# Kernel tuning notes

Hardware: AMD Instinct MI355X
Metric: run time of the kernel (lower is better)

The kernel has to match this reference:

```python
import jax, jax.numpy as jnp
import numpy as np
import math

N_EMBD = 1024
N_HEAD = 16
HEAD_DIM = N_EMBD // N_HEAD
# Faithful to source: scores = QK^T / scale, where scale = 1/sqrt(head_dim)
# => scores = QK^T * sqrt(head_dim)
INV_SCALE = math.sqrt(HEAD_DIM)


def setup_inputs() -> dict:
    key = jax.random.key(0)
    ks = jax.random.split(key, 9)
    B, S = 4, 2048
    x = jax.random.normal(ks[0], (B, S, N_EMBD), dtype=jnp.float32)
    init = 1.0 / math.sqrt(N_EMBD)
    def lin(kw, kb):
        W = jax.random.uniform(kw, (N_EMBD, N_EMBD), jnp.float32, -init, init)
        b = jax.random.uniform(kb, (N_EMBD,), jnp.float32, -init, init)
        return W, b
    Wq, bq = lin(ks[1], ks[2])
    Wk, bk = lin(ks[3], ks[4])
    Wv, bv = lin(ks[5], ks[6])
    Wo, bo = lin(ks[7], ks[8])
    return {"x": x, "Wq": Wq, "bq": bq, "Wk": Wk, "bk": bk,
            "Wv": Wv, "bv": bv, "Wo": Wo, "bo": bo}


def reference(x, Wq, bq, Wk, bk, Wv, bv, Wo, bo):
    B, S, _ = x.shape
    # projections (torch Linear: y = x @ W^T + b; here weights stored [in,out])
    q = (x @ Wq + bq).reshape(B, S, N_HEAD, HEAD_DIM)
    k = (x @ Wk + bk).reshape(B, S, N_HEAD, HEAD_DIM)
    v = (x @ Wv + bv).reshape(B, S, N_HEAD, HEAD_DIM)
    # scores: [B, H, S, S]; note unusual scaling (divide by 1/sqrt(d))
    scores = jnp.einsum('bqhd,bkhd->bhqk', q, k) * INV_SCALE
    attn = jax.nn.softmax(scores, axis=-1)
    # dropout in eval mode -> identity
    out = jnp.einsum('bhqk,bkhd->bqhd', attn, v).reshape(B, S, N_EMBD)
    return out @ Wo + bo
```

## Files before the change

kernel.cpp:

```cpp
#include <hip/hip_runtime.h>
#include <hip/hip_bf16.h>

#define DEVI static __device__ __forceinline__

typedef __attribute__((ext_vector_type(8))) _Float16 f16x8;
typedef __attribute__((ext_vector_type(2))) __fp16 fp16v2;
typedef __attribute__((ext_vector_type(4))) float f32x4;
typedef __attribute__((ext_vector_type(16))) float f32x16;
typedef __attribute__((ext_vector_type(8))) unsigned short u16x8;
typedef __attribute__((ext_vector_type(4))) unsigned int u32x4;
typedef __attribute__((ext_vector_type(2))) unsigned int u32x2;
typedef unsigned short u16;

constexpr int NE = 1024;
constexpr int NH = 16;
constexpr int HD = 64;
constexpr int SB = 4;
constexpr int SS = 2048;
constexpr int MR = SB * SS;

DEVI u16 f2h(float f) {
  union { _Float16 h; u16 u; } x;
  x.h = (_Float16)f;
  return x.u;
}

DEVI unsigned pk2(float lo, float hi) {
  union { fp16v2 h2; unsigned u; } cv;
  cv.h2 = __builtin_amdgcn_cvt_pkrtz(lo, hi);
  return cv.u;
}

DEVI void gload_lds16(const void* g, void* l) {
  __builtin_amdgcn_global_load_lds(
      (const __attribute__((address_space(1))) unsigned int*)g,
      (__attribute__((address_space(3))) unsigned int*)l, 16, 0, 0);
}

__global__ void k_cvt_x(const float* __restrict__ x, u16* __restrict__ xb) {
  size_t i = (size_t)blockIdx.x * 256 + threadIdx.x;
  const f32x4* s4 = (const f32x4*)x;
  f32x4 a = s4[2 * i], c = s4[2 * i + 1];
  u16x8 o;
  o[0] = f2h(a[0]); o[1] = f2h(a[1]); o[2] = f2h(a[2]); o[3] = f2h(a[3]);
  o[4] = f2h(c[0]); o[5] = f2h(c[1]); o[6] = f2h(c[2]); o[7] = f2h(c[3]);
  ((u16x8*)xb)[i] = o;
}

__global__ void k_wt(const float* __restrict__ W0, const float* __restrict__ W1,
                     const float* __restrict__ W2, const float* __restrict__ W3,
                     u16* __restrict__ WT) {
  __shared__ float tile[64][65];
  const float* W = (blockIdx.z == 0) ? W0 : (blockIdx.z == 1) ? W1 : (blockIdx.z == 2) ? W2 : W3;
  u16* T = WT + (size_t)blockIdx.z * NE * NE;
  int tid = threadIdx.x, c = tid & 63, rr = tid >> 6;
  int ti = blockIdx.y * 64, tj = blockIdx.x * 64;
#pragma unroll
  for (int p = 0; p < 16; p++) {
    int r = p * 4 + rr;
    tile[r][c] = W[(size_t)(ti + r) * NE + tj + c];
  }
  __syncthreads();
#pragma unroll
  for (int p = 0; p < 16; p++) {
    int r = p * 4 + rr;
    T[(size_t)(tj + r) * NE + ti + c] = f2h(tile[c][r]);
  }
}

template <int MODE>
__global__ __launch_bounds__(256) void k_gemm(const u16* __restrict__ A,
                                              const u16* __restrict__ BT,
                                              const float* __restrict__ bias,
                                              void* __restrict__ outp) {
  __shared__ __align__(16) u16 lA[128 * 64];
  __shared__ __align__(16) u16 lB[128 * 64];
  const int tid = threadIdx.x;
  const int wave = tid >> 6, lane = tid & 63;
  const int wr = wave >> 1, wc = wave & 1;
  const int fr = lane & 15, fg = lane >> 4;
  const int srow = lane >> 3;
  const int scol = ((lane & 7) ^ srow) * 8;
  const int mb = blockIdx.x, nb = blockIdx.y;
  f32x4 acc[4][4] = {};
  for (int kt = 0; kt < NE / 64; ++kt) {
#pragma unroll
    for (int p = 0; p < 4; p++) {
      int rb = wave * 32 + p * 8;
      gload_lds16(A + (size_t)(mb * 128 + rb + srow) * NE + kt * 64 + scol, lA + rb * 64);
      gload_lds16(BT + (size_t)(nb * 128 + rb + srow) * NE + kt * 64 + scol, lB + rb * 64);
    }
    __syncthreads();
#pragma unroll
    for (int kd = 0; kd < 2; ++kd) {
      f16x8 af[4], bg[4];
#pragma unroll
      for (int mi = 0; mi < 4; mi++) {
        int row = wr * 64 + mi * 16 + fr;
        af[mi] = *(const f16x8*)((const char*)lA + row * 128 + ((kd * 64 + fg * 16) ^ ((row & 7) << 4)));
      }
#pragma unroll
      for (int nj = 0; nj < 4; nj++) {
        int row = wc * 64 + nj * 16 + fr;
        bg[nj] = *(const f16x8*)((const char*)lB + row * 128 + ((kd * 64 + fg * 16) ^ ((row & 7) << 4)));
      }
#pragma unroll
      for (int mi = 0; mi < 4; mi++)
#pragma unroll
        for (int nj = 0; nj < 4; nj++)
          acc[mi][nj] = __builtin_amdgcn_mfma_f32_16x16x32_f16(af[mi], bg[nj], acc[mi][nj], 0, 0, 0);
    }
    __syncthreads();
  }
  float bv[4];
#pragma unroll
  for (int nj = 0; nj < 4; nj++) bv[nj] = bias[nb * 128 + wc * 64 + nj * 16 + fr];
#pragma unroll
  for (int mi = 0; mi < 4; mi++)
#pragma unroll
    for (int nj = 0; nj < 4; nj++)
#pragma unroll
      for (int r = 0; r < 4; r++) {
        int row = mb * 128 + wr * 64 + mi * 16 + fg * 4 + r;
        int col = nb * 128 + wc * 64 + nj * 16 + fr;
        float v = acc[mi][nj][r] + bv[nj];
        if constexpr (MODE == 2) {
          ((float*)outp)[(size_t)row * NE + col] = v;
        } else if constexpr (MODE == 0) {
          ((u16*)outp)[(size_t)row * NE + col] = f2h(v);
        } else {
          int b = row >> 11, s = row & (SS - 1);
          int h = col >> 6, d = col & 63;
          ((u16*)outp)[(((size_t)(b * NH + h) * HD + d) << 11) | (size_t)s] = f2h(v);
        }
      }
}

__global__ __launch_bounds__(256) void k_attn(const u16* __restrict__ Q, const u16* __restrict__ K,
                                              const u16* __restrict__ VT, u16* __restrict__ AO) {
  __shared__ __align__(16) u16 smem[6 * 4096];
  const int tid = threadIdx.x, wave = tid >> 6, lane = tid & 63;
  const int q32 = lane & 31, hh = lane >> 5;
  const int srow = lane >> 3;
  const int scol = ((lane & 7) ^ srow) * 8;
  const int bid = blockIdx.x;
  const int xcd = bid & 7, idx = bid >> 3;
  const int g = xcd * 8 + (idx >> 4);
  const int qb = (idx & 15) * 128;
  const int b = g >> 4, h = g & 15;
  const u16* Kg = K + (size_t)(b * SS) * NE + h * HD;
  const u16* Vg = VT + (size_t)(b * NH + h) * HD * SS;
  const u16* Qp = Q + (size_t)(b * SS + qb + wave * 32 + q32) * NE + h * HD;
  f16x8 qf[4];
#pragma unroll
  for (int m = 0; m < 4; m++) qf[m] = *(const f16x8*)(Qp + m * 16 + hh * 8);
  f32x16 oacc[2] = {};
  float m_s = -1e30f, l_s = 0.f;
  const float SC = 8.0f * 1.44269504088896340736f;

  auto STAGE = [&](int kt2, int bufi) {
    u16* lk = smem + bufi * 4096;
    u16* lv = smem + 12288 + bufi * 4096;
#pragma unroll
    for (int p = 0; p < 2; p++) {
      int rb = wave * 16 + p * 8;
      gload_lds16(Kg + (size_t)(kt2 * 64 + rb + srow) * NE + scol, lk + rb * 64);
      gload_lds16(Vg + (size_t)(rb + srow) * SS + kt2 * 64 + scol, lv + rb * 64);
    }
  };

  auto QK = [&](int bufi, f32x16* s) {
    const u16* lk = smem + bufi * 4096;
#pragma unroll
    for (int kt32 = 0; kt32 < 2; kt32++) {
      f32x16 z = {};
      int row = kt32 * 32 + q32;
      __builtin_amdgcn_s_setprio(1);
#pragma unroll
      for (int m = 0; m < 4; m++) {
        f16x8 kf = *(const f16x8*)((const char*)lk + row * 128 + ((m * 32 + hh * 16) ^ ((row & 7) << 4)));
        z = __builtin_amdgcn_mfma_f32_32x32x16_f16(kf, qf[m], z, 0, 0, 0);
      }
      __builtin_amdgcn_s_setprio(0);
      s[kt32] = z;
    }
  };

  auto SMPV = [&](int bufiV, f32x16* s) {
    const u16* lv = smem + 12288 + bufiV * 4096;
    float a[16];
#pragma unroll
    for (int r = 0; r < 16; r++) a[r] = fmaxf(s[0][r], s[1][r]);
#pragma unroll
    for (int st = 8; st > 0; st >>= 1)
#pragma unroll
      for (int r = 0; r < st; r++) a[r] = fmaxf(a[r], a[r + st]);
    float mx = a[0] * SC;
    mx = fmaxf(mx, __shfl_xor(mx, 32));
    float mo = m_s, mu = mo;
    if (!__all(mx <= mo + 8.f)) {
      float nm = fmaxf(mo, mx);
      float fs = __builtin_amdgcn_exp2f(mo - nm);
      m_s = nm; mu = nm; l_s *= fs;
#pragma unroll
      for (int d2 = 0; d2 < 2; d2++)
#pragma unroll
        for (int r = 0; r < 16; r++) oacc[d2][r] *= fs;
    }
    float p[2][16];
#pragma unroll
    for (int kt32 = 0; kt32 < 2; kt32++)
#pragma unroll
      for (int r = 0; r < 16; r++)
        p[kt32][r] = __builtin_amdgcn_exp2f(s[kt32][r] * SC - mu);
    float t[16];
#pragma unroll
    for (int r = 0; r < 16; r++) t[r] = p[0][r] + p[1][r];
#pragma unroll
    for (int st = 8; st > 0; st >>= 1)
#pragma unroll
      for (int r = 0; r < st; r++) t[r] += t[r + st];
    float rs = t[0];
    rs += __shfl_xor(rs, 32);
    l_s += rs;
    unsigned bw[4][4];
#pragma unroll
    for (int kt32 = 0; kt32 < 2; kt32++)
#pragma unroll
      for (int tau = 0; tau < 2; tau++)
#pragma unroll
        for (int b2 = 0; b2 < 2; b2++) {
          unsigned Y = pk2(p[kt32][4 * (2 * tau) + 2 * b2],     p[kt32][4 * (2 * tau) + 2 * b2 + 1]);
          unsigned X = pk2(p[kt32][4 * (2 * tau + 1) + 2 * b2], p[kt32][4 * (2 * tau + 1) + 2 * b2 + 1]);
          u32x2 r2 = __builtin_amdgcn_permlane32_swap(Y, X, false, false);
          int tt = kt32 * 2 + tau;
          bw[tt][b2]     = r2[0];
          bw[tt][b2 + 2] = r2[1];
        }
    f16x8 pf[4];
#pragma unroll
    for (int tt = 0; tt < 4; tt++) {
      union { unsigned w[4]; f16x8 v; } u;
#pragma unroll
      for (int w = 0; w < 4; w++) u.w[w] = bw[tt][w];
      pf[tt] = u.v;
    }
#pragma unroll
    for (int d2 = 0; d2 < 2; d2++) {
      int row = d2 * 32 + q32;
      __builtin_amdgcn_s_setprio(1);
#pragma unroll
      for (int tt = 0; tt < 4; tt++) {
        f16x8 vf = *(const f16x8*)((const char*)lv + row * 128 + ((tt * 32 + hh * 16) ^ ((row & 7) << 4)));
        oacc[d2] = __builtin_amdgcn_mfma_f32_32x32x16_f16(vf, pf[tt], oacc[d2], 0, 0, 0);
      }
      __builtin_amdgcn_s_setprio(0);
    }
  };

  f32x16 s[2];
  STAGE(0, 0);
  STAGE(1, 1);
  for (int kt = 0; kt < 32; ++kt) {
    const int cur = kt % 3;
    if (kt < 30) asm volatile("s_waitcnt vmcnt(4)" ::: "memory");
    else         asm volatile("s_waitcnt vmcnt(0)" ::: "memory");
    __builtin_amdgcn_s_barrier();
    __builtin_amdgcn_sched_barrier(0);
    if (kt + 2 < 32) STAGE(kt + 2, (kt + 2) % 3);
    QK(cur, s);
    SMPV(cur, s);
  }

  __syncthreads();
  unsigned* epi = (unsigned*)smem + wave * (32 * 36);
  float inv = 1.0f / l_s;
#pragma unroll
  for (int d2 = 0; d2 < 2; d2++)
#pragma unroll
    for (int aa = 0; aa < 4; aa++)
#pragma unroll
      for (int b2 = 0; b2 < 2; b2++) {
        int r0 = 4 * aa + 2 * b2;
        epi[q32 * 36 + d2 * 16 + 4 * aa + 2 * hh + b2] =
            pk2(oacc[d2][r0] * inv, oacc[d2][r0 + 1] * inv);
      }
  __syncthreads();
  {
    int q2 = lane >> 1, part = lane & 1;
    const unsigned* src = (const unsigned*)smem + wave * (32 * 36) + q2 * 36 + part * 16;
    u16* dst = AO + (size_t)(b * SS + qb + wave * 32 + q2) * NE + h * HD + part * 32;
#pragma unroll
    for (int u = 0; u < 4; u++)
      *(u32x4*)(dst + u * 8) = *(const u32x4*)(src + u * 4);
  }
}

extern "C" void kernel_launch(void* const* d_in, const int* in_sizes, int n_in,
                              void* d_out, int out_size, void* d_ws, size_t ws_size,
                              hipStream_t stream) {
  const float* x  = (const float*)d_in[0];
  const float* Wq = (const float*)d_in[1]; const float* bq = (const float*)d_in[2];
  const float* Wk = (const float*)d_in[3]; const float* bk = (const float*)d_in[4];
  const float* Wv = (const float*)d_in[5]; const float* bv = (const float*)d_in[6];
  const float* Wo = (const float*)d_in[7]; const float* bo = (const float*)d_in[8];

  u16* xb  = (u16*)d_ws;
  u16* WT  = xb  + (size_t)MR * NE;
  u16* Qb  = WT  + (size_t)4 * NE * NE;
  u16* Kb  = Qb  + (size_t)MR * NE;
  u16* VTb = Kb  + (size_t)MR * NE;
  u16* AOb = xb;

  k_cvt_x<<<dim3(MR * NE / (256 * 8)), 256, 0, stream>>>(x, xb);
  k_wt<<<dim3(16, 16, 4), 256, 0, stream>>>(Wq, Wk, Wv, Wo, WT);

  dim3 gg(MR / 128, NE / 128);
  k_gemm<0><<<gg, 256, 0, stream>>>(xb, WT + 0 * (size_t)NE * NE, bq, Qb);
  k_gemm<0><<<gg, 256, 0, stream>>>(xb, WT + 1 * (size_t)NE * NE, bk, Kb);
  k_gemm<1><<<gg, 256, 0, stream>>>(xb, WT + 2 * (size_t)NE * NE, bv, VTb);

  k_attn<<<dim3(1024), 256, 0, stream>>>(Qb, Kb, VTb, AOb);

  k_gemm<2><<<gg, 256, 0, stream>>>(AOb, WT + 3 * (size_t)NE * NE, bo, (float*)d_out);
}
```

Before: 225.0 us.

## Fuse QKV projections into one GEMM launch and read K/V directly from global

The three Q/K/V projection GEMMs become a single launch with a 24-column grid, where each block picks its bias and output buffer by segment. This removes two kernel launches and gives more blocks per wave. The attention kernel drops its LDS triple-buffered K/V staging pipeline and loads K and V fragments straight from global memory inside the MFMA loops, keeping LDS only for the epilogue. That removes barriers and LDS traffic, but it exposes global-memory latency and loses the cross-wave sharing of K/V tiles.

After: 371.5 us. 65.1% more time.

```diff
diff --git a/kernel.cpp b/kernel.cpp
--- a/kernel.cpp
+++ b/kernel.cpp
@@ -123,26 +123,88 @@
       for (int r = 0; r < 4; r++) {
         int row = mb * 128 + wr * 64 + mi * 16 + fg * 4 + r;
         int col = nb * 128 + wc * 64 + nj * 16 + fr;
-        float v = acc[mi][nj][r] + bv[nj];
-        if constexpr (MODE == 2) {
-          ((float*)outp)[(size_t)row * NE + col] = v;
-        } else if constexpr (MODE == 0) {
-          ((u16*)outp)[(size_t)row * NE + col] = f2h(v);
+        ((float*)outp)[(size_t)row * NE + col] = acc[mi][nj][r] + bv[nj];
+      }
+}
+
+__global__ __launch_bounds__(256) void k_gemm_qkv(const u16* __restrict__ A,
+                                                  const u16* __restrict__ BT,
+                                                  const float* __restrict__ bq,
+                                                  const float* __restrict__ bk,
+                                                  const float* __restrict__ bv,
+                                                  u16* __restrict__ Qb,
+                                                  u16* __restrict__ Kb,
+                                                  u16* __restrict__ VTb) {
+  __shared__ __align__(16) u16 lA[128 * 64];
+  __shared__ __align__(16) u16 lB[128 * 64];
+  const int tid = threadIdx.x;
+  const int wave = tid >> 6, lane = tid & 63;
+  const int wr = wave >> 1, wc = wave & 1;
+  const int fr = lane & 15, fg = lane >> 4;
+  const int srow = lane >> 3;
+  const int scol = ((lane & 7) ^ srow) * 8;
+  const int mb = blockIdx.x, nb = blockIdx.y;
+  const int seg = nb >> 3;
+  const float* bias = (seg == 0) ? bq : (seg == 1) ? bk : bv;
+  u16* outO = (seg == 0) ? Qb : (seg == 1) ? Kb : VTb;
+  f32x4 acc[4][4] = {};
+  for (int kt = 0; kt < NE / 64; ++kt) {
+#pragma unroll
+    for (int p = 0; p < 4; p++) {
+      int rb = wave * 32 + p * 8;
+      gload_lds16(A + (size_t)(mb * 128 + rb + srow) * NE + kt * 64 + scol, lA + rb * 64);
+      gload_lds16(BT + (size_t)(nb * 128 + rb + srow) * NE + kt * 64 + scol, lB + rb * 64);
+    }
+    __syncthreads();
+#pragma unroll
+    for (int kd = 0; kd < 2; ++kd) {
+      f16x8 af[4], bg[4];
+#pragma unroll
+      for (int mi = 0; mi < 4; mi++) {
+        int row = wr * 64 + mi * 16 + fr;
+        af[mi] = *(const f16x8*)((const char*)lA + row * 128 + ((kd * 64 + fg * 16) ^ ((row & 7) << 4)));
+      }
+#pragma unroll
+      for (int nj = 0; nj < 4; nj++) {
+        int row = wc * 64 + nj * 16 + fr;
+        bg[nj] = *(const f16x8*)((const char*)lB + row * 128 + ((kd * 64 + fg * 16) ^ ((row & 7) << 4)));
+      }
+#pragma unroll
+      for (int mi = 0; mi < 4; mi++)
+#pragma unroll
+        for (int nj = 0; nj < 4; nj++)
+          acc[mi][nj] = __builtin_amdgcn_mfma_f32_16x16x32_f16(af[mi], bg[nj], acc[mi][nj], 0, 0, 0);
+    }
+    __syncthreads();
+  }
+  const int colb = (nb & 7) * 128;
+  float bvv[4];
+#pragma unroll
+  for (int nj = 0; nj < 4; nj++) bvv[4 - 4 + nj] = bias[colb + wc * 64 + nj * 16 + fr];
+#pragma unroll
+  for (int mi = 0; mi < 4; mi++)
+#pragma unroll
+    for (int nj = 0; nj < 4; nj++)
+#pragma unroll
+      for (int r = 0; r < 4; r++) {
+        int row = mb * 128 + wr * 64 + mi * 16 + fg * 4 + r;
+        int col = colb + wc * 64 + nj * 16 + fr;
+        float v = acc[mi][nj][r] + bvv[nj];
+        if (seg < 2) {
+          outO[(size_t)row * NE + col] = f2h(v);
         } else {
           int b = row >> 11, s = row & (SS - 1);
           int h = col >> 6, d = col & 63;
-          ((u16*)outp)[(((size_t)(b * NH + h) * HD + d) << 11) | (size_t)s] = f2h(v);
+          outO[(((size_t)(b * NH + h) * HD + d) << 11) | (size_t)s] = f2h(v);
         }
       }
 }
 
 __global__ __launch_bounds__(256) void k_attn(const u16* __restrict__ Q, const u16* __restrict__ K,
                                               const u16* __restrict__ VT, u16* __restrict__ AO) {
-  __shared__ __align__(16) u16 smem[6 * 4096];
+  __shared__ unsigned epi_s[4][32 * 36];
   const int tid = threadIdx.x, wave = tid >> 6, lane = tid & 63;
   const int q32 = lane & 31, hh = lane >> 5;
-  const int srow = lane >> 3;
-  const int scol = ((lane & 7) ^ srow) * 8;
   const int bid = blockIdx.x;
   const int xcd = bid & 7, idx = bid >> 3;
   const int g = xcd * 8 + (idx >> 4);
@@ -157,37 +219,24 @@
   f32x16 oacc[2] = {};
   float m_s = -1e30f, l_s = 0.f;
   const float SC = 8.0f * 1.44269504088896340736f;
-
-  auto STAGE = [&](int kt2, int bufi) {
-    u16* lk = smem + bufi * 4096;
-    u16* lv = smem + 12288 + bufi * 4096;
-#pragma unroll
-    for (int p = 0; p < 2; p++) {
-      int rb = wave * 16 + p * 8;
-      gload_lds16(Kg + (size_t)(kt2 * 64 + rb + srow) * NE + scol, lk + rb * 64);
-      gload_lds16(Vg + (size_t)(rb + srow) * SS + kt2 * 64 + scol, lv + rb * 64);
-    }
-  };
-
-  auto QK = [&](int bufi, f32x16* s) {
-    const u16* lk = smem + bufi * 4096;
+  const u16* Kp = Kg + (size_t)q32 * NE + hh * 8;
+  const u16* Vp0 = Vg + (size_t)q32 * SS + hh * 8;
+
+  for (int kt = 0; kt < 32; ++kt) {
+    f32x16 s[2];
 #pragma unroll
     for (int kt32 = 0; kt32 < 2; kt32++) {
       f32x16 z = {};
-      int row = kt32 * 32 + q32;
+      const u16* kp = Kp + (size_t)(kt * 64 + kt32 * 32) * NE;
       __builtin_amdgcn_s_setprio(1);
 #pragma unroll
       for (int m = 0; m < 4; m++) {
-        f16x8 kf = *(const f16x8*)((const char*)lk + row * 128 + ((m * 32 + hh * 16) ^ ((row & 7) << 4)));
+        f16x8 kf = *(const f16x8*)(kp + m * 16);
         z = __builtin_amdgcn_mfma_f32_32x32x16_f16(kf, qf[m], z, 0, 0, 0);
       }
       __builtin_amdgcn_s_setprio(0);
       s[kt32] = z;
     }
-  };
-
-  auto SMPV = [&](int bufiV, f32x16* s) {
-    const u16* lv = smem + 12288 + bufiV * 4096;
     float a[16];
 #pragma unroll
     for (int r = 0; r < 16; r++) a[r] = fmaxf(s[0][r], s[1][r]);
@@ -247,33 +296,18 @@
     }
 #pragma unroll
     for (int d2 = 0; d2 < 2; d2++) {
-      int row = d2 * 32 + q32;
+      const u16* vp = Vp0 + (size_t)(d2 * 32) * SS + kt * 64;
       __builtin_amdgcn_s_setprio(1);
 #pragma unroll
       for (int tt = 0; tt < 4; tt++) {
-        f16x8 vf = *(const f16x8*)((const char*)lv + row * 128 + ((tt * 32 + hh * 16) ^ ((row & 7) << 4)));
+        f16x8 vf = *(const f16x8*)(vp + tt * 16);
         oacc[d2] = __builtin_amdgcn_mfma_f32_32x32x16_f16(vf, pf[tt], oacc[d2], 0, 0, 0);
       }
       __builtin_amdgcn_s_setprio(0);
     }
-  };
-
-  f32x16 s[2];
-  STAGE(0, 0);
-  STAGE(1, 1);
-  for (int kt = 0; kt < 32; ++kt) {
-    const int cur = kt % 3;
-    if (kt < 30) asm volatile("s_waitcnt vmcnt(4)" ::: "memory");
-    else         asm volatile("s_waitcnt vmcnt(0)" ::: "memory");
-    __builtin_amdgcn_s_barrier();
-    __builtin_amdgcn_sched_barrier(0);
-    if (kt + 2 < 32) STAGE(kt + 2, (kt + 2) % 3);
-    QK(cur, s);
-    SMPV(cur, s);
-  }
-
-  __syncthreads();
-  unsigned* epi = (unsigned*)smem + wave * (32 * 36);
+  }
+
+  unsigned* epi = &epi_s[wave][0];
   float inv = 1.0f / l_s;
 #pragma unroll
   for (int d2 = 0; d2 < 2; d2++)
@@ -285,10 +319,10 @@
         epi[q32 * 36 + d2 * 16 + 4 * aa + 2 * hh + b2] =
             pk2(oacc[d2][r0] * inv, oacc[d2][r0 + 1] * inv);
       }
-  __syncthreads();
+  __builtin_amdgcn_s_barrier();
   {
     int q2 = lane >> 1, part = lane & 1;
-    const unsigned* src = (const unsigned*)smem + wave * (32 * 36) + q2 * 36 + part * 16;
+    const unsigned* src = &epi_s[wave][0] + q2 * 36 + part * 16;
     u16* dst = AO + (size_t)(b * SS + qb + wave * 32 + q2) * NE + h * HD + part * 32;
 #pragma unroll
     for (int u = 0; u < 4; u++)
@@ -315,12 +349,9 @@
   k_cvt_x<<<dim3(MR * NE / (256 * 8)), 256, 0, stream>>>(x, xb);
   k_wt<<<dim3(16, 16, 4), 256, 0, stream>>>(Wq, Wk, Wv, Wo, WT);
 
-  dim3 gg(MR / 128, NE / 128);
-  k_gemm<0><<<gg, 256, 0, stream>>>(xb, WT + 0 * (size_t)NE * NE, bq, Qb);
-  k_gemm<0><<<gg, 256, 0, stream>>>(xb, WT + 1 * (size_t)NE * NE, bk, Kb);
-  k_gemm<1><<<gg, 256, 0, stream>>>(xb, WT + 2 * (size_t)NE * NE, bv, VTb);
+  k_gemm_qkv<<<dim3(MR / 128, 24), 256, 0, stream>>>(xb, WT, bq, bk, bv, Qb, Kb, VTb);
 
   k_attn<<<dim3(1024), 256, 0, stream>>>(Qb, Kb, VTb, AOb);
 
-  k_gemm<2><<<gg, 256, 0, stream>>>(AOb, WT + 3 * (size_t)NE * NE, bo, (float*)d_out);
-}
+  k_gemm<2><<<dim3(MR / 128, NE / 128), 256, 0, stream>>>(AOb, WT + 3 * (size_t)NE * NE, bo, (float*)d_out);
+}
```
